# Performance work log

Hardware: AMD Instinct MI355X
Metric: run time of the kernel (lower is better)

## Reference

```python
import jax, jax.numpy as jnp
import numpy as np

X_SCALE, X_ZP = 0.03, -66      # int8 quant params (qmin=-128, qmax=127)
Y_SCALE, Y_ZP = 0.025, 160     # uint8 quant params (qmin=0, qmax=255)
M = K = N = 4096


def setup_inputs() -> dict:
    key = jax.random.key(0)
    kx, ky = jax.random.split(key)
    # x holds int8-range values [-128, 127], y holds uint8-range values [0, 255]
    x = jax.random.randint(kx, (M, K), -128, 128, dtype=jnp.int32)
    y = jax.random.randint(ky, (K, N), 0, 256, dtype=jnp.int32)
    return {"x": x, "y": y}


def reference(x, y):
    # dequantize_per_tensor: (q - zero_point) * scale  (values already in [qmin, qmax])
    xf = (x.astype(jnp.float32) - X_ZP) * X_SCALE   # [M, K]
    yf = (y.astype(jnp.float32) - Y_ZP) * Y_SCALE   # [K, N]
    return jnp.matmul(xf, yf)                       # [M, N]
```

## Files before the change

kernel.cpp:

```cpp
#include <hip/hip_runtime.h>
#include <stdint.h>

#define Mdim 4096
#define Kdim 4096
#define Ndim 4096

typedef __attribute__((ext_vector_type(4))) int v4i;
typedef __attribute__((ext_vector_type(16))) int v16i;

__device__ __forceinline__ void gload_lds16(const void* g, void* l) {
  __builtin_amdgcn_global_load_lds(
      (__attribute__((address_space(1))) void*)(uintptr_t)g,
      (__attribute__((address_space(3))) void*)(uint32_t)(uintptr_t)l,
      16, 0, 0);
}

__global__ __launch_bounds__(512) void pack_fused_kernel(
    const int* __restrict__ x, const int* __restrict__ y,
    char* __restrict__ x8, char* __restrict__ yt, int* __restrict__ rsx,
    int* __restrict__ csy) {
  __shared__ int shm[512 * 5];
  const int t = threadIdx.x;
  if (blockIdx.x < 256) {
    const int n0 = blockIdx.x * 16;
    const int n = t >> 5;
    const int kq = t & 31;
    const int colw = n >> 2;
    const int byi = (n & 3) * 8;
    int bsum = 0;
#pragma unroll 1
    for (int c = 0; c < 8; ++c) {
      const int k0 = c * 512;
#pragma unroll
      for (int p = 0; p < 4; ++p) {
        const int r = (t >> 2) + p * 128;
        int4 v = *(const int4*)(y + (size_t)(k0 + r) * Ndim + n0 + (t & 3) * 4);
        int wd = (v.x & 0xff) | ((v.y & 0xff) << 8) | ((v.z & 0xff) << 16) |
                 (v.w << 24);
        shm[r * 5 + (t & 3)] = wd ^ 0x80808080;
      }
      __syncthreads();
      int outw[4];
#pragma unroll
      for (int j = 0; j < 4; ++j) {
        int b[4];
#pragma unroll
        for (int jj = 0; jj < 4; ++jj) {
          const int word = shm[(kq * 16 + j * 4 + jj) * 5 + colw];
          b[jj] = (word >> byi) & 0xff;
          bsum += (int)(char)b[jj];
        }
        outw[j] = b[0] | (b[1] << 8) | (b[2] << 16) | (b[3] << 24);
      }
      *(int4*)(yt + (size_t)(n0 + n) * Kdim + k0 + kq * 16) =
          make_int4(outw[0], outw[1], outw[2], outw[3]);
      __syncthreads();
    }
    bsum += __shfl_xor(bsum, 1, 64);
    bsum += __shfl_xor(bsum, 2, 64);
    bsum += __shfl_xor(bsum, 4, 64);
    bsum += __shfl_xor(bsum, 8, 64);
    bsum += __shfl_xor(bsum, 16, 64);
    if (kq == 0) csy[n0 + n] = bsum;
  } else {
    const int rowp = (int)(blockIdx.x - 256) * 2;
    const int h = t >> 8;
    const int tt = t & 255;
    const int row = rowp + h;
    const int4* src = (const int4*)(x + (size_t)row * Kdim);
    int4* dst = (int4*)(x8 + (size_t)row * Kdim);
    int sum = 0;
    int wd[4];
#pragma unroll
    for (int i = 0; i < 4; ++i) {
      int4 v = src[tt * 4 + i];
      sum += v.x + v.y + v.z + v.w;
      wd[i] = (v.x & 0xff) | ((v.y & 0xff) << 8) | ((v.z & 0xff) << 16) |
              (v.w << 24);
    }
    dst[tt] = make_int4(wd[0], wd[1], wd[2], wd[3]);
#pragma unroll
    for (int o = 32; o > 0; o >>= 1) sum += __shfl_down(sum, o, 64);
    if ((t & 63) == 0) shm[t >> 6] = sum;
    __syncthreads();
    if (t == 0) rsx[rowp] = shm[0] + shm[1] + shm[2] + shm[3];
    if (t == 256) rsx[rowp + 1] = shm[4] + shm[5] + shm[6] + shm[7];
  }
}

__global__ __launch_bounds__(256, 2) void gemm_i8_kernel(
    const char* __restrict__ A, const char* __restrict__ B,
    const int* __restrict__ rsx, const int* __restrict__ csy,
    float* __restrict__ out) {
  __shared__ __align__(16) char lds[3 * 24576];
  const int t = threadIdx.x;
  const int l = t & 63;
  const int w = t >> 6;
  const int warow = w >> 1;
  const int wbcol = w & 1;
  const int bm = blockIdx.y * 128;
  const int bn = blockIdx.x * 256;

  v16i acc[2][4];
#pragma unroll
  for (int i = 0; i < 2; ++i)
#pragma unroll
    for (int j = 0; j < 4; ++j)
#pragma unroll
      for (int q = 0; q < 16; ++q) acc[i][j][q] = 0;

  const int srow = t >> 2;
  const int cswz = ((t & 3) ^ ((t >> 3) & 3)) * 16;
  const char* gA = A + (size_t)(bm + srow) * Kdim + cswz;
  const char* gB = B + (size_t)(bn + srow) * Kdim + cswz;

#define STAGE(buf_off, koff)                                                  \
  do {                                                                        \
    _Pragma("unroll") for (int i = 0; i < 2; ++i)                             \
        gload_lds16(gA + (koff) + (size_t)i * 64 * Kdim,                      \
                    lds + (buf_off) + i * 4096 + t * 16);                     \
    _Pragma("unroll") for (int i = 0; i < 4; ++i)                             \
        gload_lds16(gB + (koff) + (size_t)i * 64 * Kdim,                      \
                    lds + (buf_off) + 8192 + i * 4096 + t * 16);              \
  } while (0)

  const int arow = warow * 64 + (l & 31);
  const int brow = wbcol * 128 + (l & 31);
  const int lhalf = l >> 5;
  const int lkey = (l >> 1) & 3;

#define MFMA(a, b, c) __builtin_amdgcn_mfma_i32_32x32x32_i8(a, b, c, 0, 0, 0)
#define SETP(n) __builtin_amdgcn_s_setprio(n)
#define BAR()                                                                 \
  do {                                                                        \
    asm volatile("" ::: "memory");                                            \
    __builtin_amdgcn_s_barrier();                                             \
    asm volatile("" ::: "memory");                                            \
  } while (0)
#define WAITV(n) asm volatile("s_waitcnt vmcnt(" #n ")" ::: "memory")

#define COMPUTE(buf_off)                                                      \
  do {                                                                        \
    const char* As = lds + (buf_off);                                         \
    const char* Bs = lds + (buf_off) + 8192;                                  \
    SETP(1);                                                                  \
    _Pragma("unroll") for (int ks = 0; ks < 2; ++ks) {                        \
      const int slot = ((ks * 2 + lhalf) ^ lkey) * 16;                        \
      v4i a[2], b[4];                                                         \
      _Pragma("unroll") for (int i = 0; i < 2; ++i)                           \
          a[i] = *(const v4i*)(As + (arow + i * 32) * 64 + slot);             \
      _Pragma("unroll") for (int j = 0; j < 4; ++j)                           \
          b[j] = *(const v4i*)(Bs + (brow + j * 32) * 64 + slot);             \
      _Pragma("unroll") for (int i = 0; i < 2; ++i)                           \
          _Pragma("unroll") for (int j = 0; j < 4; ++j)                       \
              acc[i][j] = MFMA(a[i], b[j], acc[i][j]);                        \
    }                                                                         \
    SETP(0);                                                                  \
  } while (0)

  STAGE(0, 0);
  STAGE(24576, 64);
  STAGE(49152, 128);
  WAITV(12);
  BAR();

#pragma unroll 1
  for (int kt = 0; kt < 60; kt += 3) {
    COMPUTE(0);
    BAR();
    STAGE(0, (kt + 3) * 64);
    WAITV(12);
    BAR();
    COMPUTE(24576);
    BAR();
    STAGE(24576, (kt + 4) * 64);
    WAITV(12);
    BAR();
    COMPUTE(49152);
    BAR();
    STAGE(49152, (kt + 5) * 64);
    WAITV(12);
    BAR();
  }
  COMPUTE(0);
  BAR();
  STAGE(0, 63 * 64);
  WAITV(12);
  BAR();
  COMPUTE(24576);
  BAR();
  WAITV(6);
  BAR();
  COMPUTE(49152);
  BAR();
  WAITV(0);
  BAR();
  COMPUTE(0);

  const int col = l & 31;
#pragma unroll
  for (int i = 0; i < 2; ++i) {
    const int gm0 = bm + warow * 64 + i * 32;
#pragma unroll
    for (int j = 0; j < 4; ++j) {
      const int gn = bn + wbcol * 128 + j * 32 + col;
      const int cs = 66 * csy[gn] - 8650752;
#pragma unroll
      for (int r = 0; r < 16; ++r) {
        const int row = (r & 3) + 8 * (r >> 2) + 4 * lhalf;
        const int gm = gm0 + row;
        const int val = acc[i][j][r] - 32 * rsx[gm] + cs;
        out[(size_t)gm * Ndim + gn] = 7.5e-4f * (float)val;
      }
    }
  }
#undef STAGE
#undef COMPUTE
#undef MFMA
#undef SETP
#undef BAR
#undef WAITV
}

extern "C" void kernel_launch(void* const* d_in, const int* in_sizes, int n_in,
                              void* d_out, int out_size, void* d_ws, size_t ws_size,
                              hipStream_t stream) {
  (void)in_sizes; (void)n_in; (void)out_size; (void)ws_size;
  const int* x = (const int*)d_in[0];
  const int* y = (const int*)d_in[1];
  float* out = (float*)d_out;
  char* ws = (char*)d_ws;
  char* x8 = ws;
  char* yt = ws + (size_t)Mdim * Kdim;
  int* rsx = (int*)(ws + (size_t)Mdim * Kdim + (size_t)Kdim * Ndim);
  int* csy = rsx + Mdim;

  pack_fused_kernel<<<256 + Mdim / 2, 512, 0, stream>>>(x, y, x8, yt, rsx, csy);
  gemm_i8_kernel<<<dim3(Ndim / 256, Mdim / 128), 256, 0, stream>>>(x8, yt, rsx,
                                                                   csy, out);
}
```

Measured before the change: 251.9 us.

## Restructure int8 GEMM to 256x256 tiles with 16x16x64 MFMA and phased pipeline

```diff
diff --git a/kernel.cpp b/kernel.cpp
--- a/kernel.cpp
+++ b/kernel.cpp
@@ -6,7 +6,6 @@
 #define Ndim 4096
 
 typedef __attribute__((ext_vector_type(4))) int v4i;
-typedef __attribute__((ext_vector_type(16))) int v16i;
 
 __device__ __forceinline__ void gload_lds16(const void* g, void* l) {
   __builtin_amdgcn_global_load_lds(
@@ -88,49 +87,49 @@
   }
 }
 
-__global__ __launch_bounds__(256, 2) void gemm_i8_kernel(
+__global__ __launch_bounds__(512, 1) void gemm_i8_kernel(
     const char* __restrict__ A, const char* __restrict__ B,
     const int* __restrict__ rsx, const int* __restrict__ csy,
     float* __restrict__ out) {
-  __shared__ __align__(16) char lds[3 * 24576];
+  __shared__ __align__(16) char lds[2 * 65536];
   const int t = threadIdx.x;
   const int l = t & 63;
   const int w = t >> 6;
   const int warow = w >> 1;
   const int wbcol = w & 1;
-  const int bm = blockIdx.y * 128;
+  const int bm = blockIdx.y * 256;
   const int bn = blockIdx.x * 256;
 
-  v16i acc[2][4];
-#pragma unroll
-  for (int i = 0; i < 2; ++i)
-#pragma unroll
-    for (int j = 0; j < 4; ++j)
-#pragma unroll
-      for (int q = 0; q < 16; ++q) acc[i][j][q] = 0;
-
-  const int srow = t >> 2;
-  const int cswz = ((t & 3) ^ ((t >> 3) & 3)) * 16;
+  v4i acc[4][8];
+#pragma unroll
+  for (int m = 0; m < 4; ++m)
+#pragma unroll
+    for (int n = 0; n < 8; ++n)
+#pragma unroll
+      for (int q = 0; q < 4; ++q) acc[m][n][q] = 0;
+
+  const int srow = t >> 3;
+  const int cswz = ((t & 7) ^ (srow & 7)) * 16;
   const char* gA = A + (size_t)(bm + srow) * Kdim + cswz;
   const char* gB = B + (size_t)(bn + srow) * Kdim + cswz;
 
-#define STAGE(buf_off, koff)                                                  \
-  do {                                                                        \
-    _Pragma("unroll") for (int i = 0; i < 2; ++i)                             \
-        gload_lds16(gA + (koff) + (size_t)i * 64 * Kdim,                      \
-                    lds + (buf_off) + i * 4096 + t * 16);                     \
-    _Pragma("unroll") for (int i = 0; i < 4; ++i)                             \
-        gload_lds16(gB + (koff) + (size_t)i * 64 * Kdim,                      \
-                    lds + (buf_off) + 8192 + i * 4096 + t * 16);              \
-  } while (0)
-
-  const int arow = warow * 64 + (l & 31);
-  const int brow = wbcol * 128 + (l & 31);
-  const int lhalf = l >> 5;
-  const int lkey = (l >> 1) & 3;
-
-#define MFMA(a, b, c) __builtin_amdgcn_mfma_i32_32x32x32_i8(a, b, c, 0, 0, 0)
+#define STG(sbo, koff, part, pass)                                            \
+  gload_lds16(((part) ? gB : gA) + (koff) + (size_t)(pass) * 64 * Kdim,       \
+              lds + (sbo) + (part) * 32768 + (pass) * 8192 + t * 16)
+
+  const int lq = l >> 4;
+  const int lk = l & 7;
+  const int sl0 = (((0 + lq) ^ lk) << 4);
+  const int sl1 = (((4 + lq) ^ lk) << 4);
+  const int abase = (warow * 64 + (l & 15)) * 128;
+  const int bbase = 32768 + (wbcol * 128 + (l & 15)) * 128;
+
+  v4i fa0[4], fa1[4];
+
+#define MFMA(a, b, c) __builtin_amdgcn_mfma_i32_16x16x64_i8(a, b, c, 0, 0, 0)
 #define SETP(n) __builtin_amdgcn_s_setprio(n)
+#define FENCE() __builtin_amdgcn_sched_barrier(0)
+#define LGKM0() asm volatile("s_waitcnt lgkmcnt(0)" ::: "memory")
 #define BAR()                                                                 \
   do {                                                                        \
     asm volatile("" ::: "memory");                                            \
@@ -139,85 +138,89 @@
   } while (0)
 #define WAITV(n) asm volatile("s_waitcnt vmcnt(" #n ")" ::: "memory")
 
-#define COMPUTE(buf_off)                                                      \
+#define PHASE(bo, n0_, RDA, sbo, koff, DOSTAGE, SP, SQ, SR, SS, TAILW)        \
   do {                                                                        \
-    const char* As = lds + (buf_off);                                         \
-    const char* Bs = lds + (buf_off) + 8192;                                  \
-    SETP(1);                                                                  \
-    _Pragma("unroll") for (int ks = 0; ks < 2; ++ks) {                        \
-      const int slot = ((ks * 2 + lhalf) ^ lkey) * 16;                        \
-      v4i a[2], b[4];                                                         \
-      _Pragma("unroll") for (int i = 0; i < 2; ++i)                           \
-          a[i] = *(const v4i*)(As + (arow + i * 32) * 64 + slot);             \
-      _Pragma("unroll") for (int j = 0; j < 4; ++j)                           \
-          b[j] = *(const v4i*)(Bs + (brow + j * 32) * 64 + slot);             \
-      _Pragma("unroll") for (int i = 0; i < 2; ++i)                           \
-          _Pragma("unroll") for (int j = 0; j < 4; ++j)                       \
-              acc[i][j] = MFMA(a[i], b[j], acc[i][j]);                        \
+    if (RDA) {                                                                \
+      _Pragma("unroll") for (int m = 0; m < 4; ++m) {                         \
+        fa0[m] = *(const v4i*)(lds + (bo) + abase + m * 2048 + sl0);          \
+        fa1[m] = *(const v4i*)(lds + (bo) + abase + m * 2048 + sl1);          \
+      }                                                                       \
     }                                                                         \
-    SETP(0);                                                                  \
+    {                                                                         \
+      v4i b00 = *(const v4i*)(lds + (bo) + bbase + (n0_)*2048 + sl0);         \
+      v4i b01 = *(const v4i*)(lds + (bo) + bbase + ((n0_) + 1) * 2048 + sl0); \
+      v4i b10 = *(const v4i*)(lds + (bo) + bbase + (n0_)*2048 + sl1);         \
+      v4i b11 = *(const v4i*)(lds + (bo) + bbase + ((n0_) + 1) * 2048 + sl1); \
+      if (DOSTAGE) {                                                          \
+        STG(sbo, koff, SP, SQ);                                               \
+        STG(sbo, koff, SR, SS);                                               \
+      }                                                                       \
+      BAR();                                                                  \
+      LGKM0();                                                                \
+      FENCE();                                                                \
+      SETP(1);                                                                \
+      _Pragma("unroll") for (int m = 0; m < 4; ++m) {                         \
+        acc[m][(n0_)] = MFMA(fa0[m], b00, acc[m][(n0_)]);                     \
+        acc[m][(n0_)] = MFMA(fa1[m], b10, acc[m][(n0_)]);                     \
+        acc[m][(n0_) + 1] = MFMA(fa0[m], b01, acc[m][(n0_) + 1]);             \
+        acc[m][(n0_) + 1] = MFMA(fa1[m], b11, acc[m][(n0_) + 1]);             \
+      }                                                                       \
+      SETP(0);                                                                \
+      FENCE();                                                                \
+      TAILW;                                                                  \
+      BAR();                                                                  \
+    }                                                                         \
   } while (0)
 
-  STAGE(0, 0);
-  STAGE(24576, 64);
-  STAGE(49152, 128);
-  WAITV(12);
-  BAR();
-
-#pragma unroll 1
-  for (int kt = 0; kt < 60; kt += 3) {
-    COMPUTE(0);
-    BAR();
-    STAGE(0, (kt + 3) * 64);
-    WAITV(12);
-    BAR();
-    COMPUTE(24576);
-    BAR();
-    STAGE(24576, (kt + 4) * 64);
-    WAITV(12);
-    BAR();
-    COMPUTE(49152);
-    BAR();
-    STAGE(49152, (kt + 5) * 64);
-    WAITV(12);
-    BAR();
-  }
-  COMPUTE(0);
-  BAR();
-  STAGE(0, 63 * 64);
-  WAITV(12);
-  BAR();
-  COMPUTE(24576);
-  BAR();
-  WAITV(6);
-  BAR();
-  COMPUTE(49152);
-  BAR();
+#define TILE(bo, sbo, koff, DOSTAGE, W1, W3)                                  \
+  do {                                                                        \
+    PHASE(bo, 0, 1, sbo, koff, DOSTAGE, 0, 0, 0, 1, (void)0);                 \
+    PHASE(bo, 2, 0, sbo, koff, DOSTAGE, 0, 2, 0, 3, W1);                      \
+    PHASE(bo, 4, 0, sbo, koff, DOSTAGE, 1, 0, 1, 2, (void)0);                 \
+    PHASE(bo, 6, 0, sbo, koff, DOSTAGE, 1, 1, 1, 3, W3);                      \
+  } while (0)
+
+#pragma unroll
+  for (int p = 0; p < 4; ++p) STG(0, 0, 0, p);
+#pragma unroll
+  for (int p = 0; p < 4; ++p) STG(0, 0, 1, p);
   WAITV(0);
   BAR();
-  COMPUTE(0);
-
-  const int col = l & 31;
-#pragma unroll
-  for (int i = 0; i < 2; ++i) {
-    const int gm0 = bm + warow * 64 + i * 32;
-#pragma unroll
-    for (int j = 0; j < 4; ++j) {
-      const int gn = bn + wbcol * 128 + j * 32 + col;
+
+#pragma unroll 1
+  for (int kt = 0; kt < 30; kt += 2) {
+    TILE(0, 65536, (kt + 1) * 128, 1, WAITV(4), WAITV(2));
+    TILE(65536, 0, (kt + 2) * 128, 1, WAITV(4), WAITV(2));
+  }
+  TILE(0, 65536, 31 * 128, 1, WAITV(4), WAITV(2));
+  TILE(65536, 0, 0, 0, WAITV(0), (void)0);
+
+  const int col = l & 15;
+  const int r4 = lq * 4;
+#pragma unroll
+  for (int m = 0; m < 4; ++m) {
+    const int gm0 = bm + warow * 64 + m * 16 + r4;
+    int rsv[4];
+#pragma unroll
+    for (int r = 0; r < 4; ++r) rsv[r] = 32 * rsx[gm0 + r];
+#pragma unroll
+    for (int n = 0; n < 8; ++n) {
+      const int gn = bn + wbcol * 128 + n * 16 + col;
       const int cs = 66 * csy[gn] - 8650752;
 #pragma unroll
-      for (int r = 0; r < 16; ++r) {
-        const int row = (r & 3) + 8 * (r >> 2) + 4 * lhalf;
-        const int gm = gm0 + row;
-        const int val = acc[i][j][r] - 32 * rsx[gm] + cs;
-        out[(size_t)gm * Ndim + gn] = 7.5e-4f * (float)val;
+      for (int r = 0; r < 4; ++r) {
+        const int val = acc[m][n][r] - rsv[r] + cs;
+        out[(size_t)(gm0 + r) * Ndim + gn] = 7.5e-4f * (float)val;
       }
     }
   }
-#undef STAGE
-#undef COMPUTE
+#undef STG
+#undef PHASE
+#undef TILE
 #undef MFMA
 #undef SETP
+#undef FENCE
+#undef LGKM0
 #undef BAR
 #undef WAITV
 }
@@ -236,6 +239,6 @@
   int* csy = rsx + Mdim;
 
   pack_fused_kernel<<<256 + Mdim / 2, 512, 0, stream>>>(x, y, x8, yt, rsx, csy);
-  gemm_i8_kernel<<<dim3(Ndim / 256, Mdim / 128), 256, 0, stream>>>(x8, yt, rsx,
+  gemm_i8_kernel<<<dim3(Ndim / 256, Mdim / 256), 512, 0, stream>>>(x8, yt, rsx,
                                                                    csy, out);
 }
```

New measurement: 236.4 us. -6.2%, faster.
